# Kernel tuning notes

Measured on AMD Instinct MI355X. Metric: run time of the kernel, lower is better.

Reference implementation:

```python
import jax, jax.numpy as jnp
import numpy as np

NEG_SLOPE = 0.2
N, IN_DIM, OUT_DIM, N_HEADS = 4096, 512, 512, 4
D_K = OUT_DIM // N_HEADS


def setup_inputs() -> dict:
    key = jax.random.key(0)
    k1, k2, k3, k4, k5 = jax.random.split(key, 5)
    H = jax.random.normal(k1, (N, IN_DIM), dtype=jnp.float32)
    A = jax.random.randint(k2, (N, N), 0, 2, dtype=jnp.int32)
    W = jax.random.normal(k3, (IN_DIM, OUT_DIM), dtype=jnp.float32) * (1.0 / np.sqrt(IN_DIM))
    a_l = jax.random.normal(k4, (N_HEADS, D_K), dtype=jnp.float32) * 0.1
    a_r = jax.random.normal(k5, (N_HEADS, D_K), dtype=jnp.float32) * 0.1
    return {"H": H, "A": A, "W": W, "a_l": a_l, "a_r": a_r}


def reference(H, A, W, a_l, a_r):
    n = H.shape[0]
    # mask = (A + I) > 0, shape (N, N); self-loops always allowed
    mask = (A + jnp.eye(n, dtype=A.dtype)) > 0
    # Wh: (N, heads, d_k)
    Wh = (H @ W).reshape(n, N_HEADS, D_K)
    sl = jnp.einsum('nhd,hd->nh', Wh, a_l)  # (N, heads)
    sr = jnp.einsum('nhd,hd->nh', Wh, a_r)  # (N, heads)
    # e[i, h, j] = leaky_relu(sl[i,h] + sr[j,h])
    e = jax.nn.leaky_relu(sl[:, :, None] + sr.T[None, :, :], negative_slope=NEG_SLOPE)
    e = jnp.where(mask[:, None, :], e, -jnp.inf)
    alpha = jnp.nan_to_num(jax.nn.softmax(e, axis=2), nan=0.0)  # dropout is identity at eval
    # out[i, h, :] = sum_j alpha[i,h,j] * Wh[j,h,:]
    out = jnp.einsum('nhm,mhd->nhd', alpha, Wh).reshape(n, OUT_DIM)
    return jax.nn.elu(out)
```

## Files before the change

kernel.cpp:

```cpp
#include <hip/hip_runtime.h>

typedef unsigned short ushort_t;
typedef __attribute__((ext_vector_type(8)))  short  short8;
typedef __attribute__((ext_vector_type(4)))  short  short4v;
typedef __attribute__((ext_vector_type(4)))  float  float4v;
typedef __attribute__((ext_vector_type(4)))  int    int4v;

#define N_NODES 4096
#define NHEADS  4
#define DK      128
#define ODIM    512
#define KDIM    512

__device__ __forceinline__ float bf2f(ushort_t u) {
    return __uint_as_float(((unsigned)u) << 16);
}
__device__ __forceinline__ ushort_t f2bf_rne(float f) {
    unsigned u = __float_as_uint(f);
    u += 0x7fffu + ((u >> 16) & 1u);
    return (ushort_t)(u >> 16);
}

__global__ __launch_bounds__(256) void pack_mask_k(const int* __restrict__ A,
                                                   unsigned long long* __restrict__ P,
                                                   const ushort_t* __restrict__ Hraw,
                                                   int* __restrict__ flag,
                                                   const void* __restrict__ W,
                                                   ushort_t* __restrict__ WT,
                                                   float* __restrict__ sl,
                                                   float* __restrict__ sr)
{
    __shared__ ushort_t lt[64][72];
    __shared__ int dcnt[4];
    const int tid = threadIdx.x;
    const int bx  = blockIdx.x;

    if (bx == 0 && tid < 64) {
        const int lane = tid;
        int cnt = 0;
        #pragma unroll
        for (int s = 0; s < 16; ++s) {
            ushort_t v = Hraw[(lane * 16 + s) * 2];
            int e = (v >> 7) & 0xFF;
            cnt += (((e >= 90) && (e <= 140)) || (v == 0)) ? 1 : 0;
        }
        #pragma unroll
        for (int off = 32; off; off >>= 1) cnt += __shfl_down(cnt, off);
        if (lane == 0) *flag = (cnt < 768) ? 1 : 0;
    }

    {
        const int lane  = tid & 63;
        const int flat4 = bx * 256 + tid;
        const int row   = flat4 >> 10;
        const int col0  = (flat4 << 2) & 4095;
        const int4v a   = ((const int4v*)A)[flat4];
        unsigned nib = 0;
        #pragma unroll
        for (int j = 0; j < 4; ++j)
            nib |= ((a[j] != 0) || (row == col0 + j)) ? (1u << j) : 0u;
        unsigned long long v = (unsigned long long)nib << ((lane & 15) * 4);
        v |= __shfl_xor(v, 1);
        v |= __shfl_xor(v, 2);
        v |= __shfl_xor(v, 4);
        v |= __shfl_xor(v, 8);
        if ((lane & 15) == 0) P[flat4 >> 4] = v;
    }

    if (bx >= 64 && bx < 96) {
        const int idx = (bx - 64) * 256 + tid;
        float4v z;
        #pragma unroll
        for (int e = 0; e < 4; ++e) z[e] = 0.f;
        if (idx < 4096) ((float4v*)sl)[idx] = z;
        else            ((float4v*)sr)[idx - 4096] = z;
    }

    if (bx < 64) {
        int cnt = 0;
        #pragma unroll
        for (int s = 0; s < 4; ++s) {
            ushort_t v = Hraw[(tid * 4 + s) * 2];
            int e = (v >> 7) & 0xFF;
            cnt += (((e >= 90) && (e <= 140)) || (v == 0)) ? 1 : 0;
        }
        #pragma unroll
        for (int off = 32; off; off >>= 1) cnt += __shfl_down(cnt, off);
        if ((tid & 63) == 0) dcnt[tid >> 6] = cnt;
        __syncthreads();
        const int f32 = (dcnt[0] + dcnt[1] + dcnt[2] + dcnt[3]) < 768;

        const int ti = bx >> 3, tj = bx & 7;
        const int r = tid >> 2, c2 = tid & 3;
        const size_t eo = (size_t)(ti * 64 + r) * KDIM + tj * 64 + c2 * 16;
        if (f32) {
            const float4v* src = (const float4v*)((const float*)W + eo);
            float4v f0 = src[0], f1 = src[1], f2 = src[2], f3 = src[3];
            #pragma unroll
            for (int e = 0; e < 4; ++e) {
                lt[r][c2 * 16 +  0 + e] = f2bf_rne(f0[e]);
                lt[r][c2 * 16 +  4 + e] = f2bf_rne(f1[e]);
                lt[r][c2 * 16 +  8 + e] = f2bf_rne(f2[e]);
                lt[r][c2 * 16 + 12 + e] = f2bf_rne(f3[e]);
            }
        } else {
            const short8* src = (const short8*)((const ushort_t*)W + eo);
            short8 v0 = src[0];
            short8 v1 = src[1];
            *(short8*)&lt[r][c2 * 16]     = v0;
            *(short8*)&lt[r][c2 * 16 + 8] = v1;
        }
        __syncthreads();
        #pragma unroll
        for (int itr = 0; itr < 2; ++itr) {
            int idx = itr * 256 + tid;
            int n = idx >> 3, c = idx & 7;
            short8 vv;
            #pragma unroll
            for (int e = 0; e < 8; ++e) vv[e] = (short)lt[c * 8 + e][n];
            *(short8*)(WT + (size_t)(tj * 64 + n) * KDIM + ti * 64 + c * 8) = vv;
        }
    }
}

__global__ __launch_bounds__(256) void gemm_wht_dual_k(const void* __restrict__ H,
                                                       const ushort_t* __restrict__ WT,
                                                       ushort_t* __restrict__ WhT,
                                                       const int* __restrict__ flag,
                                                       const void* __restrict__ al,
                                                       const void* __restrict__ ar,
                                                       float* __restrict__ sl,
                                                       float* __restrict__ sr)
{
    __shared__ ushort_t lt[64][72];
    const int f32 = *flag;
    const int tid  = threadIdx.x;
    const int lane = tid & 63;
    const int wid  = tid >> 6;
    const int quad = lane >> 4;
    const int l15  = lane & 15;
    const int bm = blockIdx.x & 63, bn = blockIdx.x >> 6;
    const int i0 = bm * 64, n0 = bn * 64;

    const size_t aoff = (size_t)(i0 + wid * 16 + l15) * KDIM + quad * 8;
    const short8* bp0 = (const short8*)(WT + (size_t)(n0 +  0 + l15) * KDIM) + quad;
    const short8* bp1 = (const short8*)(WT + (size_t)(n0 + 16 + l15) * KDIM) + quad;
    const short8* bp2 = (const short8*)(WT + (size_t)(n0 + 32 + l15) * KDIM) + quad;
    const short8* bp3 = (const short8*)(WT + (size_t)(n0 + 48 + l15) * KDIM) + quad;

    float4v acc0, acc1, acc2, acc3;
    #pragma unroll
    for (int e = 0; e < 4; ++e) { acc0[e] = 0.f; acc1[e] = 0.f; acc2[e] = 0.f; acc3[e] = 0.f; }

    #pragma unroll 4
    for (int k8 = 0; k8 < 64; k8 += 4) {
        short8 a;
        if (f32) {
            const float4v* fp = (const float4v*)((const float*)H + aoff + (size_t)k8 * 8);
            float4v x0 = fp[0], x1 = fp[1];
            #pragma unroll
            for (int e = 0; e < 4; ++e) {
                a[e]     = (short)f2bf_rne(x0[e]);
                a[4 + e] = (short)f2bf_rne(x1[e]);
            }
        } else {
            a = *(const short8*)((const ushort_t*)H + aoff + (size_t)k8 * 8);
        }
        acc0 = __builtin_amdgcn_mfma_f32_16x16x32_bf16(a, bp0[k8], acc0, 0, 0, 0);
        acc1 = __builtin_amdgcn_mfma_f32_16x16x32_bf16(a, bp1[k8], acc1, 0, 0, 0);
        acc2 = __builtin_amdgcn_mfma_f32_16x16x32_bf16(a, bp2[k8], acc2, 0, 0, 0);
        acc3 = __builtin_amdgcn_mfma_f32_16x16x32_bf16(a, bp3[k8], acc3, 0, 0, 0);
    }

    #pragma unroll
    for (int r = 0; r < 4; ++r) {
        int m = wid * 16 + quad * 4 + r;
        lt[ 0 + l15][m] = f2bf_rne(acc0[r]);
        lt[16 + l15][m] = f2bf_rne(acc1[r]);
        lt[32 + l15][m] = f2bf_rne(acc2[r]);
        lt[48 + l15][m] = f2bf_rne(acc3[r]);
    }
    __syncthreads();
    #pragma unroll
    for (int itr = 0; itr < 2; ++itr) {
        int idx = itr * 256 + tid;
        int n = idx >> 3, c = idx & 7;
        short8 v = *(const short8*)&lt[n][c * 8];
        *(short8*)(WhT + (size_t)(n0 + n) * N_NODES + i0 + c * 8) = v;
    }

    {
        const int h2 = n0 >> 7;
        const int d0 = n0 & 127;
        const int m  = tid >> 2;
        const int part = tid & 3;
        float psl = 0.f, psr = 0.f;
        #pragma unroll
        for (int k = 0; k < 16; ++k) {
            int n = part * 16 + k;
            float wv = bf2f(lt[n][m]);
            float av = f32 ? ((const float*)al)[h2 * DK + d0 + n]
                           : bf2f(((const ushort_t*)al)[h2 * DK + d0 + n]);
            float bv = f32 ? ((const float*)ar)[h2 * DK + d0 + n]
                           : bf2f(((const ushort_t*)ar)[h2 * DK + d0 + n]);
            psl += wv * av;
            psr += wv * bv;
        }
        psl += __shfl_down(psl, 2); psl += __shfl_down(psl, 1);
        psr += __shfl_down(psr, 2); psr += __shfl_down(psr, 1);
        if (part == 0) {
            atomicAdd(&sl[h2 * N_NODES + i0 + m], psl);
            atomicAdd(&sr[h2 * N_NODES + i0 + m], psr);
        }
    }
}

__global__ __launch_bounds__(256, 2) void attn_split_k(const ushort_t* __restrict__ WhT,
                                                       const unsigned* __restrict__ Apack,
                                                       const float* __restrict__ sl,
                                                       const float* __restrict__ sr,
                                                       float* __restrict__ Npart,
                                                       float* __restrict__ Dpart)
{
    __shared__ char smem[81920] __attribute__((aligned(16)));
    float*    srs  = (float*)smem;
    unsigned (*mbuf)[64] = (unsigned (*)[64])(smem + 8192);
    ushort_t* vbuf = (ushort_t*)(smem + 16384);

    const int tid  = threadIdx.x;
    const int lane = tid & 63;
    const int wq   = tid >> 6;
    const int quad = lane >> 4;
    const int l15  = lane & 15;
    const int bx   = blockIdx.x;
    const int half = bx & 1;
    const int h    = (bx >> 1) & 3;
    const int i0   = (bx >> 3) << 5;
    const int jbase = half << 11;

    const float C1 = 1.44269504f;

    for (int j = tid; j < 2048; j += 256) srs[j] = sr[h * N_NODES + jbase + j] * C1;
    for (int t = tid; t < 32 * 64; t += 256) {
        int r = t >> 6, c = t & 63;
        mbuf[r][c ^ r] = Apack[(size_t)(i0 + r) * 128 + (half << 6) + c];
    }
    const float slv0 = sl[h * N_NODES + i0 + l15] * C1;
    const float slv1 = sl[h * N_NODES + i0 + 16 + l15] * C1;
    __syncthreads();

    float4v acc[2][8];
    #pragma unroll
    for (int mg = 0; mg < 2; ++mg)
        #pragma unroll
        for (int nt = 0; nt < 8; ++nt)
            #pragma unroll
            for (int e = 0; e < 4; ++e) acc[mg][nt][e] = 0.f;
    float4v accden0, accden1;
    #pragma unroll
    for (int e = 0; e < 4; ++e) { accden0[e] = 0.f; accden1[e] = 0.f; }

    short8 ones;
    #pragma unroll
    for (int e = 0; e < 8; ++e) ones[e] = (short)0x3F80;

    const int Lrow = lane >> 2;
    const int gch  = (lane & 3) ^ ((lane >> 3) & 3);
    const ushort_t* gdma = WhT + (size_t)(h * DK + Lrow) * N_NODES + jbase + gch * 8;

    #define DMA_WIN(CUR, JW)                                                           \
        {   ushort_t* ld_ = vbuf + wq * 8192 + (CUR) * 4096;                           \
            const ushort_t* g_ = gdma + (JW);                                          \
            _Pragma("unroll")                                                          \
            for (int q_ = 0; q_ < 8; ++q_)                                             \
                __builtin_amdgcn_global_load_lds(                                      \
                    (const __attribute__((address_space(1))) void*)(g_ + (size_t)q_ * 16 * N_NODES), \
                    (__attribute__((address_space(3))) void*)(ld_ + q_ * 512),         \
                    16, 0, 0);                                                         \
        }

    DMA_WIN(0, wq * 512)
    DMA_WIN(1, wq * 512 + 32)

    const int so = (quad ^ ((l15 >> 1) & 3)) * 8;

    #pragma unroll 1
    for (int it = 0; it < 16; ++it) {
        const int cur = it & 1;
        const int jl  = wq * 512 + it * 32;
        const int mc  = jl >> 5;

        const unsigned wa = mbuf[l15][mc ^ l15];
        const unsigned wb = mbuf[16 + l15][mc ^ (16 + l15)];
        const float4v s0 = *(const float4v*)&srs[jl + quad * 8];
        const float4v s1 = *(const float4v*)&srs[jl + quad * 8 + 4];

        short8 pf0, pf1;
        #pragma unroll
        for (int jj = 0; jj < 8; ++jj) {
            float srj = (jj < 4) ? s0[jj] : s1[jj - 4];
            int bit = quad * 8 + jj;
            float x0 = slv0 + srj;
            float t0 = fmaxf(x0, x0 * 0.2f);
            t0 = ((wa >> bit) & 1u) ? t0 : -1e30f;
            pf0[jj] = (short)(ushort_t)(__float_as_uint(__builtin_amdgcn_exp2f(t0)) >> 16);
            float x1 = slv1 + srj;
            float t1 = fmaxf(x1, x1 * 0.2f);
            t1 = ((wb >> bit) & 1u) ? t1 : -1e30f;
            pf1[jj] = (short)(ushort_t)(__float_as_uint(__builtin_amdgcn_exp2f(t1)) >> 16);
        }

        if (it == 15) { asm volatile("s_waitcnt vmcnt(0)" ::: "memory"); }
        else          { asm volatile("s_waitcnt vmcnt(8)" ::: "memory"); }

        const ushort_t* vB = vbuf + wq * 8192 + cur * 4096;
        #pragma unroll
        for (int nt = 0; nt < 8; ++nt) {
            short8 b = *(const short8*)(vB + (nt * 16 + l15) * 32 + so);
            acc[0][nt] = __builtin_amdgcn_mfma_f32_16x16x32_bf16(pf0, b, acc[0][nt], 0, 0, 0);
            acc[1][nt] = __builtin_amdgcn_mfma_f32_16x16x32_bf16(pf1, b, acc[1][nt], 0, 0, 0);
        }
        accden0 = __builtin_amdgcn_mfma_f32_16x16x32_bf16(pf0, ones, accden0, 0, 0, 0);
        accden1 = __builtin_amdgcn_mfma_f32_16x16x32_bf16(pf1, ones, accden1, 0, 0, 0);

        if (it < 14) DMA_WIN(cur, wq * 512 + (it + 2) * 32)
    }
    #undef DMA_WIN

    float* red  = (float*)(smem + 16384);
    float* lsum = (float*)(smem + 32768);
    __syncthreads();

    if (l15 == 0) {
        #pragma unroll
        for (int r = 0; r < 4; ++r) {
            lsum[wq * 32 + quad * 4 + r]      = accden0[r];
            lsum[wq * 32 + 16 + quad * 4 + r] = accden1[r];
        }
    }
    #define RED_WRITE                                                                \
        { _Pragma("unroll")                                                          \
          for (int mg = 0; mg < 2; ++mg)                                             \
            _Pragma("unroll")                                                        \
            for (int nt = 0; nt < 8; ++nt)                                           \
              _Pragma("unroll")                                                      \
              for (int r = 0; r < 4; ++r)                                            \
                red[(mg * 16 + quad * 4 + r) * 128 + nt * 16 + l15] = acc[mg][nt][r]; }
    #define RED_ADD                                                                 \
        { _Pragma("unroll")                                                          \
          for (int mg = 0; mg < 2; ++mg)                                             \
            _Pragma("unroll")                                                        \
            for (int nt = 0; nt < 8; ++nt)                                           \
              _Pragma("unroll")                                                      \
              for (int r = 0; r < 4; ++r)                                            \
                acc[mg][nt][r] += red[(mg * 16 + quad * 4 + r) * 128 + nt * 16 + l15]; }

    if (wq == 1) RED_WRITE
    __syncthreads();
    if (wq == 0) RED_ADD
    __syncthreads();
    if (wq == 3) RED_WRITE
    __syncthreads();
    if (wq == 2) RED_ADD
    __syncthreads();
    if (wq == 2) RED_WRITE
    __syncthreads();
    if (wq == 0) {
        RED_ADD
        float* Np = Npart + (size_t)half * N_NODES * ODIM;
        #pragma unroll
        for (int mg = 0; mg < 2; ++mg)
            #pragma unroll
            for (int nt = 0; nt < 8; ++nt)
                #pragma unroll
                for (int r = 0; r < 4; ++r) {
                    int rowi = mg * 16 + quad * 4 + r;
                    Np[(size_t)(i0 + rowi) * ODIM + h * DK + nt * 16 + l15] = acc[mg][nt][r];
                }
        if (l15 == 0) {
            #pragma unroll
            for (int mg = 0; mg < 2; ++mg)
                #pragma unroll
                for (int r = 0; r < 4; ++r) {
                    int rowi = mg * 16 + quad * 4 + r;
                    float den = lsum[rowi] + lsum[32 + rowi] + lsum[64 + rowi] + lsum[96 + rowi];
                    Dpart[(half * 4 + h) * N_NODES + i0 + rowi] = den;
                }
        }
    }
    #undef RED_WRITE
    #undef RED_ADD
}

__global__ __launch_bounds__(256) void merge_k(const float* __restrict__ Npart,
                                               const float* __restrict__ Dpart,
                                               void* __restrict__ out,
                                               const int* __restrict__ flag)
{
    const int f32 = *flag;
    const size_t e4 = ((size_t)blockIdx.x * 256 + threadIdx.x) * 4;
    const int i = (int)(e4 >> 9);
    const int c = (int)(e4 & 511);
    const int h = c >> 7;
    const float4v n0 = *(const float4v*)(Npart + e4);
    const float4v n1 = *(const float4v*)(Npart + (size_t)N_NODES * ODIM + e4);
    const float den = Dpart[h * N_NODES + i] + Dpart[(4 + h) * N_NODES + i];
    const float rinv = 1.0f / fmaxf(den, 1e-37f);
    const float C1 = 1.44269504f;
    float o[4];
    #pragma unroll
    for (int k = 0; k < 4; ++k) {
        float v = (n0[k] + n1[k]) * rinv;
        float e = __builtin_amdgcn_exp2f(v * C1) - 1.0f;
        o[k] = (v > 0.f) ? v : e;
    }
    if (f32) {
        float4v ov;
        #pragma unroll
        for (int k = 0; k < 4; ++k) ov[k] = o[k];
        *(float4v*)((float*)out + e4) = ov;
    } else {
        short4v ov;
        #pragma unroll
        for (int k = 0; k < 4; ++k) ov[k] = (short)f2bf_rne(o[k]);
        *(short4v*)((ushort_t*)out + e4) = ov;
    }
}

__global__ __launch_bounds__(256, 2) void attn_single_k(const ushort_t* __restrict__ WhT,
                                                        const unsigned* __restrict__ Apack,
                                                        const float* __restrict__ sl,
                                                        const float* __restrict__ sr,
                                                        void* __restrict__ out,
                                                        const int* __restrict__ flag)
{
    __shared__ float    srs[N_NODES];
    __shared__ unsigned mbuf[32][128];
    __shared__ float    red[2][32][128];
    __shared__ float    lsum[4][32];

    const int f32  = *flag;
    const int tid  = threadIdx.x;
    const int lane = tid & 63;
    const int wq   = tid >> 6;
    const int quad = lane >> 4;
    const int l15  = lane & 15;
    const int h    = blockIdx.x & 3;
    const int i0   = (blockIdx.x >> 2) << 5;

    for (int j = tid; j < N_NODES; j += 256) srs[j] = sr[h * N_NODES + j];
    for (int t = tid; t < 32 * 128; t += 256) {
        int r = t >> 7, c = t & 127;
        mbuf[r][c] = Apack[(size_t)(i0 + r) * 128 + c];
    }
    const float slv0 = sl[h * N_NODES + i0 + l15];
    const float slv1 = sl[h * N_NODES + i0 + 16 + l15];
    __syncthreads();

    const float C1 = 1.44269504f;
    const float C2 = 0.2f * 1.44269504f;

    float4v acc[2][8];
    #pragma unroll
    for (int mg = 0; mg < 2; ++mg)
        #pragma unroll
        for (int nt = 0; nt < 8; ++nt)
            #pragma unroll
            for (int e = 0; e < 4; ++e) acc[mg][nt][e] = 0.f;
    float lacc0 = 0.f, lacc1 = 0.f;

    const ushort_t* vb = WhT + (size_t)(h * DK + l15) * N_NODES + wq * 1024 + quad * 8;

    #pragma unroll 1
    for (int it = 0; it < 16; ++it) {
        const int jl = it * 64;
        const int j0 = wq * 1024 + jl;
        const int mc = j0 >> 5;

        short8 bf[8][2];
        #pragma unroll
        for (int nt = 0; nt < 8; ++nt) {
            bf[nt][0] = *(const short8*)(vb + (size_t)nt * 16 * N_NODES + jl);
            bf[nt][1] = *(const short8*)(vb + (size_t)nt * 16 * N_NODES + jl + 32);
        }

        const unsigned wa0 = mbuf[l15][mc],      wa1 = mbuf[l15][mc + 1];
        const unsigned wb0 = mbuf[16 + l15][mc], wb1 = mbuf[16 + l15][mc + 1];

        short8 pf0[2], pf1[2];
        #pragma unroll
        for (int s = 0; s < 2; ++s) {
            const float* sp = &srs[j0 + s * 32 + quad * 8];
            const float4v s0 = *(const float4v*)sp;
            const float4v s1 = *(const float4v*)(sp + 4);
            const unsigned wa = s ? wa1 : wa0;
            const unsigned wb = s ? wb1 : wb0;
            #pragma unroll
            for (int jj = 0; jj < 8; ++jj) {
                float srj = (jj < 4) ? s0[jj] : s1[jj - 4];
                int bit = quad * 8 + jj;
                float x0 = slv0 + srj;
                float t0 = fmaxf(x0 * C1, x0 * C2);
                t0 = ((wa >> bit) & 1u) ? t0 : -1e30f;
                float p0 = __builtin_amdgcn_exp2f(t0);
                ushort_t h0 = (ushort_t)(__float_as_uint(p0) >> 16);
                lacc0 += bf2f(h0);
                pf0[s][jj] = (short)h0;
                float x1 = slv1 + srj;
                float t1 = fmaxf(x1 * C1, x1 * C2);
                t1 = ((wb >> bit) & 1u) ? t1 : -1e30f;
                float p1 = __builtin_amdgcn_exp2f(t1);
                ushort_t h1 = (ushort_t)(__float_as_uint(p1) >> 16);
                lacc1 += bf2f(h1);
                pf1[s][jj] = (short)h1;
            }
        }

        #pragma unroll
        for (int nt = 0; nt < 8; ++nt) {
            acc[0][nt] = __builtin_amdgcn_mfma_f32_16x16x32_bf16(pf0[0], bf[nt][0], acc[0][nt], 0, 0, 0);
            acc[0][nt] = __builtin_amdgcn_mfma_f32_16x16x32_bf16(pf0[1], bf[nt][1], acc[0][nt], 0, 0, 0);
            acc[1][nt] = __builtin_amdgcn_mfma_f32_16x16x32_bf16(pf1[0], bf[nt][0], acc[1][nt], 0, 0, 0);
            acc[1][nt] = __builtin_amdgcn_mfma_f32_16x16x32_bf16(pf1[1], bf[nt][1], acc[1][nt], 0, 0, 0);
        }
    }

    lacc0 += __shfl_xor(lacc0, 16);
    lacc0 += __shfl_xor(lacc0, 32);
    lacc1 += __shfl_xor(lacc1, 16);
    lacc1 += __shfl_xor(lacc1, 32);
    if (lane < 16) {
        lsum[wq][l15]      = lacc0;
        lsum[wq][16 + l15] = lacc1;
    }
    if (wq >= 2) {
        #pragma unroll
        for (int mg = 0; mg < 2; ++mg)
            #pragma unroll
            for (int nt = 0; nt < 8; ++nt)
                #pragma unroll
                for (int r = 0; r < 4; ++r)
                    red[wq - 2][mg * 16 + quad * 4 + r][nt * 16 + l15] = acc[mg][nt][r];
    }
    __syncthreads();
    if (wq < 2) {
        #pragma unroll
        for (int mg = 0; mg < 2; ++mg)
            #pragma unroll
            for (int nt = 0; nt < 8; ++nt)
                #pragma unroll
                for (int r = 0; r < 4; ++r)
                    acc[mg][nt][r] += red[wq][mg * 16 + quad * 4 + r][nt * 16 + l15];
    }
    __syncthreads();
    if (wq == 1) {
        #pragma unroll
        for (int mg = 0; mg < 2; ++mg)
            #pragma unroll
            for (int nt = 0; nt < 8; ++nt)
                #pragma unroll
                for (int r = 0; r < 4; ++r)
                    red[0][mg * 16 + quad * 4 + r][nt * 16 + l15] = acc[mg][nt][r];
    }
    __syncthreads();
    if (wq == 0) {
        #pragma unroll
        for (int mg = 0; mg < 2; ++mg) {
            float linv[4];
            #pragma unroll
            for (int r = 0; r < 4; ++r) {
                int rowi = mg * 16 + quad * 4 + r;
                float den = lsum[0][rowi] + lsum[1][rowi] + lsum[2][rowi] + lsum[3][rowi];
                linv[r] = 1.0f / fmaxf(den, 1e-37f);
            }
            #pragma unroll
            for (int nt = 0; nt < 8; ++nt)
                #pragma unroll
                for (int r = 0; r < 4; ++r) {
                    int rowi = mg * 16 + quad * 4 + r;
                    float v = (acc[mg][nt][r] + red[0][rowi][nt * 16 + l15]) * linv[r];
                    float e = __builtin_amdgcn_exp2f(v * C1) - 1.0f;
                    float o = (v > 0.f) ? v : e;
                    size_t oidx = (size_t)(i0 + rowi) * ODIM + h * DK + nt * 16 + l15;
                    if (f32) ((float*)out)[oidx] = o;
                    else     ((ushort_t*)out)[oidx] = f2bf_rne(o);
                }
        }
    }
}

extern "C" void kernel_launch(void* const* d_in, const int* in_sizes, int n_in,
                              void* d_out, int out_size, void* d_ws, size_t ws_size,
                              hipStream_t stream)
{
    const void* H  = d_in[0];
    const int*  A  = (const int*)d_in[1];
    const void* W  = d_in[2];
    const void* al = d_in[3];
    const void* ar = d_in[4];

    if (ws_size < (7u << 20)) return;

    char* ws = (char*)d_ws;
    ushort_t* WhT   = (ushort_t*)ws;
    unsigned long long* Apack = (unsigned long long*)(ws + (4u << 20));
    ushort_t* WT    = (ushort_t*)(ws + (6u << 20));
    float*    sl    = (float*)(ws + (6u << 20) + (512u << 10));
    float*    sr    = (float*)(ws + (6u << 20) + (576u << 10));
    int*      flag  = (int*)(ws + (6u << 20) + (640u << 10));
    float*    Npart = (float*)(ws + (12u << 20));
    float*    Dpart = (float*)(ws + (28u << 20));
    const bool have_split = ws_size >= (29u << 20);

    pack_mask_k    <<<16384, 256, 0, stream>>>(A, Apack, (const ushort_t*)H, flag,
                                               W, WT, sl, sr);
    gemm_wht_dual_k<<<512,   256, 0, stream>>>(H, WT, WhT, flag, al, ar, sl, sr);
    if (have_split) {
        attn_split_k<<<1024, 256, 0, stream>>>(WhT, (const unsigned*)Apack, sl, sr, Npart, Dpart);
        merge_k     <<<2048, 256, 0, stream>>>(Npart, Dpart, (void*)d_out, flag);
    } else {
        attn_single_k<<<512, 256, 0, stream>>>(WhT, (const unsigned*)Apack, sl, sr, (void*)d_out, flag);
    }
}
```

Baseline: 181.1 us.

## Split attention work across row groups per wave with shared triple-buffered V tiles

The attention kernel now gives each block 64 rows, and each wave owns 16 of them across the full 2048-column half. Before, each wave handled 32 rows over a quarter of the columns, so partial sums had to be reduced across waves. The V tile is now loaded cooperatively into a three-deep shared LDS ring, with a barrier per step. Each wave reuses the whole V tile, which removes the cross-wave LDS reduction and halves the grid. The cost is a block-wide barrier every iteration, and with only 512 blocks occupancy may be lower.

```diff
diff --git a/kernel.cpp b/kernel.cpp
--- a/kernel.cpp
+++ b/kernel.cpp
@@ -222,10 +222,10 @@
                                                        float* __restrict__ Npart,
                                                        float* __restrict__ Dpart)
 {
-    __shared__ char smem[81920] __attribute__((aligned(16)));
+    __shared__ char smem[73728] __attribute__((aligned(16)));
     float*    srs  = (float*)smem;
     unsigned (*mbuf)[64] = (unsigned (*)[64])(smem + 8192);
-    ushort_t* vbuf = (ushort_t*)(smem + 16384);
+    ushort_t* vbuf = (ushort_t*)(smem + 24576);
 
     const int tid  = threadIdx.x;
     const int lane = tid & 63;
@@ -235,161 +235,115 @@
     const int bx   = blockIdx.x;
     const int half = bx & 1;
     const int h    = (bx >> 1) & 3;
-    const int i0   = (bx >> 3) << 5;
+    const int i0   = (bx >> 3) << 6;
     const int jbase = half << 11;
 
     const float C1 = 1.44269504f;
 
     for (int j = tid; j < 2048; j += 256) srs[j] = sr[h * N_NODES + jbase + j] * C1;
-    for (int t = tid; t < 32 * 64; t += 256) {
+    for (int t = tid; t < 64 * 64; t += 256) {
         int r = t >> 6, c = t & 63;
         mbuf[r][c ^ r] = Apack[(size_t)(i0 + r) * 128 + (half << 6) + c];
     }
-    const float slv0 = sl[h * N_NODES + i0 + l15] * C1;
-    const float slv1 = sl[h * N_NODES + i0 + 16 + l15] * C1;
+    const int myrow = wq * 16 + l15;
+    const float slv = sl[h * N_NODES + i0 + myrow] * C1;
     __syncthreads();
 
-    float4v acc[2][8];
-    #pragma unroll
-    for (int mg = 0; mg < 2; ++mg)
-        #pragma unroll
-        for (int nt = 0; nt < 8; ++nt)
-            #pragma unroll
-            for (int e = 0; e < 4; ++e) acc[mg][nt][e] = 0.f;
-    float4v accden0, accden1;
-    #pragma unroll
-    for (int e = 0; e < 4; ++e) { accden0[e] = 0.f; accden1[e] = 0.f; }
+    float4v acc[8];
+    #pragma unroll
+    for (int nt = 0; nt < 8; ++nt)
+        #pragma unroll
+        for (int e = 0; e < 4; ++e) acc[nt][e] = 0.f;
+    float4v accden;
+    #pragma unroll
+    for (int e = 0; e < 4; ++e) accden[e] = 0.f;
 
     short8 ones;
     #pragma unroll
     for (int e = 0; e < 8; ++e) ones[e] = (short)0x3F80;
 
-    const int Lrow = lane >> 2;
-    const int gch  = (lane & 3) ^ ((lane >> 3) & 3);
-    const ushort_t* gdma = WhT + (size_t)(h * DK + Lrow) * N_NODES + jbase + gch * 8;
-
-    #define DMA_WIN(CUR, JW)                                                           \
-        {   ushort_t* ld_ = vbuf + wq * 8192 + (CUR) * 4096;                           \
-            const ushort_t* g_ = gdma + (JW);                                          \
-            _Pragma("unroll")                                                          \
-            for (int q_ = 0; q_ < 8; ++q_)                                             \
-                __builtin_amdgcn_global_load_lds(                                      \
-                    (const __attribute__((address_space(1))) void*)(g_ + (size_t)q_ * 16 * N_NODES), \
-                    (__attribute__((address_space(3))) void*)(ld_ + q_ * 512),         \
-                    16, 0, 0);                                                         \
-        }
-
-    DMA_WIN(0, wq * 512)
-    DMA_WIN(1, wq * 512 + 32)
-
-    const int so = (quad ^ ((l15 >> 1) & 3)) * 8;
+    const int dl  = lane >> 3;
+    const int pch = (lane & 7) ^ (dl & 7);
+    const ushort_t* g0 = WhT + (size_t)(h * DK + wq * 32 + dl) * N_NODES + jbase + pch * 8;
+
+    #define DMA_WIN(BUF, IW)                                                         \
+        {   ushort_t* lb_ = vbuf + (BUF) * 8192 + wq * 2048;                         \
+            const ushort_t* gs_ = g0 + (IW) * 64;                                    \
+            _Pragma("unroll")                                                        \
+            for (int q_ = 0; q_ < 4; ++q_)                                           \
+                __builtin_amdgcn_global_load_lds(                                    \
+                    (const __attribute__((address_space(1))) void*)(gs_ + (size_t)q_ * 8 * N_NODES), \
+                    (__attribute__((address_space(3))) void*)(lb_ + q_ * 512),       \
+                    16, 0, 0);                                                       \
+        }
+
+    DMA_WIN(0, 0)
+    DMA_WIN(1, 1)
+
+    const int rs0 = (quad     ^ (l15 & 7)) * 8;
+    const int rs1 = ((4 + quad) ^ (l15 & 7)) * 8;
 
     #pragma unroll 1
-    for (int it = 0; it < 16; ++it) {
-        const int cur = it & 1;
-        const int jl  = wq * 512 + it * 32;
-        const int mc  = jl >> 5;
-
-        const unsigned wa = mbuf[l15][mc ^ l15];
-        const unsigned wb = mbuf[16 + l15][mc ^ (16 + l15)];
+    for (int iw = 0; iw < 32; ++iw) {
+        const int jl = iw * 64;
+
+        const unsigned wa0 = mbuf[myrow][(iw * 2)     ^ myrow];
+        const unsigned wa1 = mbuf[myrow][(iw * 2 + 1) ^ myrow];
         const float4v s0 = *(const float4v*)&srs[jl + quad * 8];
         const float4v s1 = *(const float4v*)&srs[jl + quad * 8 + 4];
-
-        short8 pf0, pf1;
+        const float4v s2 = *(const float4v*)&srs[jl + 32 + quad * 8];
+        const float4v s3 = *(const float4v*)&srs[jl + 32 + quad * 8 + 4];
+
+        short8 pfA, pfB;
         #pragma unroll
         for (int jj = 0; jj < 8; ++jj) {
-            float srj = (jj < 4) ? s0[jj] : s1[jj - 4];
-            int bit = quad * 8 + jj;
-            float x0 = slv0 + srj;
-            float t0 = fmaxf(x0, x0 * 0.2f);
-            t0 = ((wa >> bit) & 1u) ? t0 : -1e30f;
-            pf0[jj] = (short)(ushort_t)(__float_as_uint(__builtin_amdgcn_exp2f(t0)) >> 16);
-            float x1 = slv1 + srj;
-            float t1 = fmaxf(x1, x1 * 0.2f);
-            t1 = ((wb >> bit) & 1u) ? t1 : -1e30f;
-            pf1[jj] = (short)(ushort_t)(__float_as_uint(__builtin_amdgcn_exp2f(t1)) >> 16);
-        }
-
-        if (it == 15) { asm volatile("s_waitcnt vmcnt(0)" ::: "memory"); }
-        else          { asm volatile("s_waitcnt vmcnt(8)" ::: "memory"); }
-
-        const ushort_t* vB = vbuf + wq * 8192 + cur * 4096;
+            const int bit = quad * 8 + jj;
+            float srjA = (jj < 4) ? s0[jj] : s1[jj - 4];
+            float xA = slv + srjA;
+            float tA = fmaxf(xA, xA * 0.2f);
+            tA = ((wa0 >> bit) & 1u) ? tA : -1e30f;
+            pfA[jj] = (short)(ushort_t)(__float_as_uint(__builtin_amdgcn_exp2f(tA)) >> 16);
+            float srjB = (jj < 4) ? s2[jj] : s3[jj - 4];
+            float xB = slv + srjB;
+            float tB = fmaxf(xB, xB * 0.2f);
+            tB = ((wa1 >> bit) & 1u) ? tB : -1e30f;
+            pfB[jj] = (short)(ushort_t)(__float_as_uint(__builtin_amdgcn_exp2f(tB)) >> 16);
+        }
+
+        if (iw == 31) { asm volatile("s_waitcnt vmcnt(0)" ::: "memory"); }
+        else          { asm volatile("s_waitcnt vmcnt(4)" ::: "memory"); }
+        asm volatile("s_barrier" ::: "memory");
+        if (iw < 30) DMA_WIN((iw + 2) % 3, iw + 2)
+
+        const ushort_t* vB = vbuf + (iw % 3) * 8192;
         #pragma unroll
         for (int nt = 0; nt < 8; ++nt) {
-            short8 b = *(const short8*)(vB + (nt * 16 + l15) * 32 + so);
-            acc[0][nt] = __builtin_amdgcn_mfma_f32_16x16x32_bf16(pf0, b, acc[0][nt], 0, 0, 0);
-            acc[1][nt] = __builtin_amdgcn_mfma_f32_16x16x32_bf16(pf1, b, acc[1][nt], 0, 0, 0);
-        }
-        accden0 = __builtin_amdgcn_mfma_f32_16x16x32_bf16(pf0, ones, accden0, 0, 0, 0);
-        accden1 = __builtin_amdgcn_mfma_f32_16x16x32_bf16(pf1, ones, accden1, 0, 0, 0);
-
-        if (it < 14) DMA_WIN(cur, wq * 512 + (it + 2) * 32)
+            const int d64 = (nt * 16 + l15) * 64;
+            short8 b0 = *(const short8*)(vB + d64 + rs0);
+            short8 b1 = *(const short8*)(vB + d64 + rs1);
+            acc[nt] = __builtin_amdgcn_mfma_f32_16x16x32_bf16(pfA, b0, acc[nt], 0, 0, 0);
+            acc[nt] = __builtin_amdgcn_mfma_f32_16x16x32_bf16(pfB, b1, acc[nt], 0, 0, 0);
+        }
+        accden = __builtin_amdgcn_mfma_f32_16x16x32_bf16(pfA, ones, accden, 0, 0, 0);
+        accden = __builtin_amdgcn_mfma_f32_16x16x32_bf16(pfB, ones, accden, 0, 0, 0);
     }
     #undef DMA_WIN
 
-    float* red  = (float*)(smem + 16384);
-    float* lsum = (float*)(smem + 32768);
-    __syncthreads();
-
+    float* Np = Npart + (size_t)half * N_NODES * ODIM;
+    #pragma unroll
+    for (int nt = 0; nt < 8; ++nt)
+        #pragma unroll
+        for (int r = 0; r < 4; ++r) {
+            const int rowi = wq * 16 + quad * 4 + r;
+            Np[(size_t)(i0 + rowi) * ODIM + h * DK + nt * 16 + l15] = acc[nt][r];
+        }
     if (l15 == 0) {
         #pragma unroll
         for (int r = 0; r < 4; ++r) {
-            lsum[wq * 32 + quad * 4 + r]      = accden0[r];
-            lsum[wq * 32 + 16 + quad * 4 + r] = accden1[r];
-        }
-    }
-    #define RED_WRITE                                                                \
-        { _Pragma("unroll")                                                          \
-          for (int mg = 0; mg < 2; ++mg)                                             \
-            _Pragma("unroll")                                                        \
-            for (int nt = 0; nt < 8; ++nt)                                           \
-              _Pragma("unroll")                                                      \
-              for (int r = 0; r < 4; ++r)                                            \
-                red[(mg * 16 + quad * 4 + r) * 128 + nt * 16 + l15] = acc[mg][nt][r]; }
-    #define RED_ADD                                                                 \
-        { _Pragma("unroll")                                                          \
-          for (int mg = 0; mg < 2; ++mg)                                             \
-            _Pragma("unroll")                                                        \
-            for (int nt = 0; nt < 8; ++nt)                                           \
-              _Pragma("unroll")                                                      \
-              for (int r = 0; r < 4; ++r)                                            \
-                acc[mg][nt][r] += red[(mg * 16 + quad * 4 + r) * 128 + nt * 16 + l15]; }
-
-    if (wq == 1) RED_WRITE
-    __syncthreads();
-    if (wq == 0) RED_ADD
-    __syncthreads();
-    if (wq == 3) RED_WRITE
-    __syncthreads();
-    if (wq == 2) RED_ADD
-    __syncthreads();
-    if (wq == 2) RED_WRITE
-    __syncthreads();
-    if (wq == 0) {
-        RED_ADD
-        float* Np = Npart + (size_t)half * N_NODES * ODIM;
-        #pragma unroll
-        for (int mg = 0; mg < 2; ++mg)
-            #pragma unroll
-            for (int nt = 0; nt < 8; ++nt)
-                #pragma unroll
-                for (int r = 0; r < 4; ++r) {
-                    int rowi = mg * 16 + quad * 4 + r;
-                    Np[(size_t)(i0 + rowi) * ODIM + h * DK + nt * 16 + l15] = acc[mg][nt][r];
-                }
-        if (l15 == 0) {
-            #pragma unroll
-            for (int mg = 0; mg < 2; ++mg)
-                #pragma unroll
-                for (int r = 0; r < 4; ++r) {
-                    int rowi = mg * 16 + quad * 4 + r;
-                    float den = lsum[rowi] + lsum[32 + rowi] + lsum[64 + rowi] + lsum[96 + rowi];
-                    Dpart[(half * 4 + h) * N_NODES + i0 + rowi] = den;
-                }
-        }
-    }
-    #undef RED_WRITE
-    #undef RED_ADD
+            const int rowi = wq * 16 + quad * 4 + r;
+            Dpart[(half * 4 + h) * N_NODES + i0 + rowi] = accden[r];
+        }
+    }
 }
 
 __global__ __launch_bounds__(256) void merge_k(const float* __restrict__ Npart,
@@ -616,7 +570,7 @@
                                                W, WT, sl, sr);
     gemm_wht_dual_k<<<512,   256, 0, stream>>>(H, WT, WhT, flag, al, ar, sl, sr);
     if (have_split) {
-        attn_split_k<<<1024, 256, 0, stream>>>(WhT, (const unsigned*)Apack, sl, sr, Npart, Dpart);
+        attn_split_k<<<512, 256, 0, stream>>>(WhT, (const unsigned*)Apack, sl, sr, Npart, Dpart);
         merge_k     <<<2048, 256, 0, stream>>>(Npart, Dpart, (void*)d_out, flag);
     } else {
         attn_single_k<<<512, 256, 0, stream>>>(WhT, (const unsigned*)Apack, sl, sr, (void*)d_out, flag);
```

New measurement: 174.0 us. -3.9%, faster.
